# Kernel tuning notes

Measured on AMD Instinct MI355X. Metric: run time of the kernel, lower is better.

## Reference

```python
import jax, jax.numpy as jnp
import numpy as np

NUM_GRAPHS = 128

def _gcn_conv(x, W, b, src, dst, deg_inv_sqrt, n_nodes):
    # PyG GCNConv: h = X W; out[dst] += d^-1/2[src] * d^-1/2[dst] * h[src]; out += b
    h = x @ W
    norm = deg_inv_sqrt[src] * deg_inv_sqrt[dst]  # [E]
    msg = h[src] * norm[:, None]                  # [E, C]
    out = jax.ops.segment_sum(msg, dst, num_segments=n_nodes)
    return out + b


def setup_inputs() -> dict:
    key = jax.random.key(0)
    k1, k2, k3, k4, k5 = jax.random.split(key, 5)
    n_nodes, n_edges, c_in, c_hid = 50000, 800000, 256, 256
    x = jax.random.normal(k1, (n_nodes, c_in), dtype=jnp.float32)
    edge_index = jax.random.randint(k2, (2, n_edges), 0, n_nodes, dtype=jnp.int64)
    batch = jnp.sort(jax.random.randint(k3, (n_nodes,), 0, NUM_GRAPHS, dtype=jnp.int64))
    s1 = 1.0 / np.sqrt(c_in)
    s2 = 1.0 / np.sqrt(c_hid)
    W1 = jax.random.uniform(k4, (c_in, c_hid), jnp.float32, -s1, s1)
    b1 = jnp.zeros((c_hid,), jnp.float32)
    W2 = jax.random.uniform(k5, (c_hid, c_hid), jnp.float32, -s2, s2)
    b2 = jnp.zeros((c_hid,), jnp.float32)
    return {"x": x, "edge_index": edge_index, "batch": batch,
            "W1": W1, "b1": b1, "W2": W2, "b2": b2}


def reference(x, edge_index, batch, W1, b1, W2, b2):
    n_nodes = x.shape[0]
    # add self-loops (GCNConv default add_self_loops=True)
    loops = jnp.arange(n_nodes, dtype=edge_index.dtype)
    src = jnp.concatenate([edge_index[0], loops])
    dst = jnp.concatenate([edge_index[1], loops])
    deg = jax.ops.segment_sum(jnp.ones_like(dst, dtype=x.dtype), dst, num_segments=n_nodes)
    deg_inv_sqrt = jnp.where(deg > 0, jax.lax.rsqrt(deg), 0.0)

    h = jax.nn.relu(_gcn_conv(x, W1, b1, src, dst, deg_inv_sqrt, n_nodes))
    # dropout p=0.2 is identity in eval mode
    h = jax.nn.relu(_gcn_conv(h, W2, b2, src, dst, deg_inv_sqrt, n_nodes))

    # global mean pool over graph ids
    sums = jax.ops.segment_sum(h, batch, num_segments=NUM_GRAPHS)
    cnts = jax.ops.segment_sum(jnp.ones((n_nodes,), h.dtype), batch, num_segments=NUM_GRAPHS)
    return sums / jnp.maximum(cnts, 1.0)[:, None]
```

## Files before the change

### kernel.cpp

```cpp
#include <hip/hip_runtime.h>

#define NCH 256
#define NS  16

typedef short short8 __attribute__((ext_vector_type(8)));
typedef float f32x4  __attribute__((ext_vector_type(4)));

__device__ __forceinline__ float b2f(unsigned short u) {
    union { unsigned int i; float f; } x; x.i = ((unsigned int)u) << 16; return x.f;
}
__device__ __forceinline__ unsigned short f2b(float f) {
    unsigned int u = __float_as_uint(f);
    unsigned int r = (u + 0x7FFFu + ((u >> 16) & 1u)) >> 16;
    return (unsigned short)r;
}

__global__ __launch_bounds__(256) void k_hist(const int* __restrict__ dst, int E,
                                              int* __restrict__ deg) {
    int e = blockIdx.x * 256 + threadIdx.x;
    if (e < E) atomicAdd(&deg[dst[e]], 1);
}

__global__ __launch_bounds__(256) void k_scan_blk(const int* __restrict__ deg,
                                                  int* __restrict__ part,
                                                  int* __restrict__ bsum, int N) {
    __shared__ int sm[256];
    int t = threadIdx.x;
    int base = blockIdx.x * 1024 + t * 4;
    int v[4]; int s = 0;
#pragma unroll
    for (int j = 0; j < 4; ++j) {
        int i = base + j;
        int d = (i < N) ? deg[i] : 0;
        v[j] = d; s += d;
    }
    sm[t] = s; __syncthreads();
#pragma unroll
    for (int off = 1; off < 256; off <<= 1) {
        int u = (t >= off) ? sm[t - off] : 0;
        __syncthreads();
        sm[t] += u;
        __syncthreads();
    }
    int excl = sm[t] - s;
#pragma unroll
    for (int j = 0; j < 4; ++j) {
        int i = base + j;
        if (i < N) part[i] = excl;
        excl += v[j];
    }
    if (t == 255) bsum[blockIdx.x] = sm[255];
}

__global__ void k_scan_top(int* __restrict__ bsum, int nb, int* __restrict__ rowptr_end) {
    int t = threadIdx.x;
    int orig = (t < nb) ? bsum[t] : 0;
    int v = orig;
#pragma unroll
    for (int off = 1; off < 64; off <<= 1) {
        int u = __shfl_up(v, off, 64);
        if (t >= off) v += u;
    }
    if (t < nb) bsum[t] = v - orig;
    if (t == 63) *rowptr_end = v;
}

__global__ __launch_bounds__(256) void k_finalize(const int* __restrict__ deg,
                                                  int* __restrict__ row_ptr,
                                                  const int* __restrict__ boff,
                                                  int* __restrict__ cursor,
                                                  float* __restrict__ dinv, int N) {
    int i = blockIdx.x * 256 + threadIdx.x;
    if (i < N) {
        int rp = row_ptr[i] + boff[i >> 10];
        row_ptr[i] = rp;
        cursor[i]  = rp;
        dinv[i] = rsqrtf((float)(deg[i] + 1));
    }
}

__global__ __launch_bounds__(256) void k_scatter(const int* __restrict__ src,
                                                 const int* __restrict__ dst, int E,
                                                 int* __restrict__ cursor,
                                                 const float* __restrict__ dinv,
                                                 int2* __restrict__ cw) {
    int e = blockIdx.x * 256 + threadIdx.x;
    if (e < E) {
        int d = dst[e];
        int s = src[e];
        int pos = atomicAdd(&cursor[d], 1);
        cw[pos] = make_int2(s, __float_as_int(dinv[s]));
    }
}

__global__ __launch_bounds__(256) void k_castT(const float* __restrict__ W1,
                                               const float* __restrict__ W2,
                                               unsigned short* __restrict__ Wt1,
                                               unsigned short* __restrict__ Wt2) {
    int k = blockIdx.x, n = threadIdx.x;
    const float* W = blockIdx.y ? W2 : W1;
    unsigned short* Wt = blockIdx.y ? Wt2 : Wt1;
    Wt[(size_t)n * 256 + k] = f2b(W[(size_t)k * 256 + n]);
}

__device__ __forceinline__ void a_load_b(const unsigned short* __restrict__ A,
                                         int tile, int M, int lr, int ku, short8* dst) {
    int row = tile * 16 + lr; if (row >= M) row = M - 1;
    const unsigned short* pa = A + (size_t)row * NCH + ku * 8;
#pragma unroll
    for (int ks = 0; ks < 8; ++ks) dst[ks] = *(const short8*)(pa + ks * 32);
}

__device__ __forceinline__ void a_load_f(const float* __restrict__ A,
                                         int tile, int M, int lr, int ku, short8* dst) {
    int row = tile * 16 + lr; if (row >= M) row = M - 1;
    const float* pa = A + (size_t)row * NCH + ku * 8;
#pragma unroll
    for (int ks = 0; ks < 8; ++ks) {
        float4 f0 = *(const float4*)(pa + ks * 32);
        float4 f1 = *(const float4*)(pa + ks * 32 + 4);
        short8 v;
        v[0] = (short)f2b(f0.x); v[1] = (short)f2b(f0.y);
        v[2] = (short)f2b(f0.z); v[3] = (short)f2b(f0.w);
        v[4] = (short)f2b(f1.x); v[5] = (short)f2b(f1.y);
        v[6] = (short)f2b(f1.z); v[7] = (short)f2b(f1.w);
        dst[ks] = v;
    }
}

template <bool AF32>
__device__ __forceinline__ void gemm_body(const void* __restrict__ Av,
                                          const unsigned short* __restrict__ Bt,
                                          unsigned short* __restrict__ C, int M) {
    const int tid  = threadIdx.x;
    const int wid  = tid >> 6;
    const int lane = tid & 63;
    const int lr   = lane & 15;
    const int ku   = lane >> 4;

    short8 bfr[4][8];
    {
        const unsigned short* pb = Bt + (size_t)(wid * 64 + lr) * NCH + ku * 8;
#pragma unroll
        for (int nf = 0; nf < 4; ++nf)
#pragma unroll
            for (int ks = 0; ks < 8; ++ks)
                bfr[nf][ks] = *(const short8*)(pb + nf * 16 * NCH + ks * 32);
    }

    const int tiles = (M + 15) >> 4;
    int t = blockIdx.x;

    short8 afA[8], afB[8];
    if (t < tiles) {
        if (AF32) a_load_f((const float*)Av, t, M, lr, ku, afA);
        else      a_load_b((const unsigned short*)Av, t, M, lr, ku, afA);
    }

    for (; t < tiles; t += gridDim.x) {
        int tn = t + gridDim.x;
        if (tn < tiles) {
            if (AF32) a_load_f((const float*)Av, tn, M, lr, ku, afB);
            else      a_load_b((const unsigned short*)Av, tn, M, lr, ku, afB);
        }

        f32x4 acc[4];
#pragma unroll
        for (int nf = 0; nf < 4; ++nf) acc[nf] = (f32x4){0.f, 0.f, 0.f, 0.f};

#pragma unroll
        for (int ks = 0; ks < 8; ++ks)
#pragma unroll
            for (int nf = 0; nf < 4; ++nf)
                acc[nf] = __builtin_amdgcn_mfma_f32_16x16x32_bf16(bfr[nf][ks], afA[ks],
                                                                  acc[nf], 0, 0, 0);

        int row = t * 16 + lr;
        if (row < M) {
            unsigned short* pc = C + (size_t)row * NCH + wid * 64 + ku * 4;
#pragma unroll
            for (int nf = 0; nf < 4; ++nf) {
                unsigned short us[4];
                us[0] = f2b(acc[nf][0]); us[1] = f2b(acc[nf][1]);
                us[2] = f2b(acc[nf][2]); us[3] = f2b(acc[nf][3]);
                *(int2*)(pc + nf * 16) = *(const int2*)us;
            }
        }
#pragma unroll
        for (int ks = 0; ks < 8; ++ks) afA[ks] = afB[ks];
    }
}

__global__ __launch_bounds__(256, 2) void k_gemm_f32in(const float* __restrict__ A,
                                                       const unsigned short* __restrict__ Bt,
                                                       unsigned short* __restrict__ C, int M) {
    gemm_body<true>(A, Bt, C, M);
}

__global__ __launch_bounds__(256, 2) void k_gemm_rs(const unsigned short* __restrict__ A,
                                                    const unsigned short* __restrict__ Bt,
                                                    unsigned short* __restrict__ C, int M) {
    gemm_body<false>(A, Bt, C, M);
}

__global__ __launch_bounds__(256) void k_agg_w(const unsigned short* __restrict__ h,
                                               const float* __restrict__ dinv,
                                               const int* __restrict__ row_ptr,
                                               const int2* __restrict__ cw,
                                               const float* __restrict__ bias,
                                               unsigned short* __restrict__ out,
                                               int v0, int vend) {
    int v = v0 + blockIdx.x * 4 + (threadIdx.x >> 6);
    if (v >= vend) return;
    const int lane = threadIdx.x & 63;
    const int half = lane >> 5;
    const int cb   = (lane & 31) << 3;

    float acc[8] = {};
    float dv = dinv[v];

    short8 rs = {};
    if (half == 0) rs = *(const short8*)&h[(size_t)v * NCH + cb];

    int beg = row_ptr[v], end = row_ptr[v + 1];
    int i0 = beg + half * 2;

    short8 r0 = {}, r1 = {};
    float  w0 = 0.f, w1 = 0.f;
    bool b0 = i0 < end, b1 = i0 + 1 < end;
    if (b0) {
        int2 e = cw[i0];
        r0 = *(const short8*)&h[(size_t)e.x * NCH + cb];
        w0 = __int_as_float(e.y);
    }
    if (b1) {
        int2 e = cw[i0 + 1];
        r1 = *(const short8*)&h[(size_t)e.x * NCH + cb];
        w1 = __int_as_float(e.y);
    }

    while (b0) {
        int in = i0 + 4;
        bool n0 = in < end, n1 = in + 1 < end;
        short8 s0 = {}, s1 = {};
        float  x0 = 0.f, x1 = 0.f;
        if (n0) {
            int2 e = cw[in];
            s0 = *(const short8*)&h[(size_t)e.x * NCH + cb];
            x0 = __int_as_float(e.y);
        }
        if (n1) {
            int2 e = cw[in + 1];
            s1 = *(const short8*)&h[(size_t)e.x * NCH + cb];
            x1 = __int_as_float(e.y);
        }
#pragma unroll
        for (int i = 0; i < 8; ++i) acc[i] += w0 * b2f((unsigned short)r0[i]);
#pragma unroll
        for (int i = 0; i < 8; ++i) acc[i] += w1 * b2f((unsigned short)r1[i]);
        r0 = s0; r1 = s1; w0 = x0; w1 = x1; b0 = n0; b1 = n1; i0 = in;
    }

    if (half == 0) {
#pragma unroll
        for (int i = 0; i < 8; ++i) acc[i] += dv * b2f((unsigned short)rs[i]);
    }

#pragma unroll
    for (int i = 0; i < 8; ++i) acc[i] += __shfl_xor(acc[i], 32, 64);

    if (half == 0) {
        f32x4 bl = *(const f32x4*)&bias[cb];
        f32x4 bh = *(const f32x4*)&bias[cb + 4];
        unsigned short us[8];
#pragma unroll
        for (int i = 0; i < 8; ++i) {
            float b = (i < 4) ? bl[i] : bh[i - 4];
            us[i] = f2b(fmaxf(dv * acc[i] + b, 0.0f));
        }
        *(int4*)&out[(size_t)v * NCH + cb] = *(const int4*)us;
    }
}

__device__ __forceinline__ int lower_bound_i(const int* a, int n, int key) {
    int lo = 0, hi = n;
    while (lo < hi) {
        int mid = (lo + hi) >> 1;
        if (a[mid] < key) lo = mid + 1; else hi = mid;
    }
    return lo;
}

__global__ __launch_bounds__(64) void k_pool_a(const unsigned short* __restrict__ a,
                                               const int* __restrict__ batch,
                                               float* __restrict__ partial, int N) {
    int g = blockIdx.x, s = blockIdx.y;
    const int lane = threadIdx.x;
    const int half = lane >> 5;
    const int cb   = (lane & 31) << 3;

    int lo = lower_bound_i(batch, N, g);
    int hi = lower_bound_i(batch, N, g + 1);
    int cnt = hi - lo;
    int len = (cnt + NS - 1) / NS;
    int rlo = lo + s * len;
    int rhi = min(rlo + len, hi);

    float acc[8] = {};
    for (int r = rlo + half; r < rhi; r += 2) {
        short8 hv = *(const short8*)&a[(size_t)r * NCH + cb];
#pragma unroll
        for (int i = 0; i < 8; ++i) acc[i] += b2f((unsigned short)hv[i]);
    }
#pragma unroll
    for (int i = 0; i < 8; ++i) acc[i] += __shfl_xor(acc[i], 32, 64);

    if (half == 0) {
        float* p = partial + ((size_t)g * NS + s) * NCH + cb;
        *(f32x4*)p       = (f32x4){acc[0], acc[1], acc[2], acc[3]};
        *(f32x4*)(p + 4) = (f32x4){acc[4], acc[5], acc[6], acc[7]};
    }
}

__global__ __launch_bounds__(256) void k_pool_b(const float* __restrict__ partial,
                                                const int* __restrict__ batch,
                                                float* __restrict__ out, int N) {
    int g = blockIdx.x, ch = threadIdx.x;
    int lo = lower_bound_i(batch, N, g);
    int hi = lower_bound_i(batch, N, g + 1);
    float s = 0.0f;
#pragma unroll
    for (int k = 0; k < NS; ++k)
        s += partial[((size_t)g * NS + k) * NCH + ch];
    out[(size_t)g * NCH + ch] = s / (float)max(hi - lo, 1);
}

extern "C" void kernel_launch(void* const* d_in, const int* in_sizes, int n_in,
                              void* d_out, int out_size, void* d_ws, size_t ws_size,
                              hipStream_t stream) {
    const float* x     = (const float*)d_in[0];
    const int*   ei    = (const int*)d_in[1];
    const int*   batch = (const int*)d_in[2];
    const float* W1    = (const float*)d_in[3];
    const float* b1    = (const float*)d_in[4];
    const float* W2    = (const float*)d_in[5];
    const float* b2    = (const float*)d_in[6];
    float* out = (float*)d_out;

    const int M = in_sizes[0] / NCH;
    const int E = in_sizes[1] / 2;
    const int* src = ei;
    const int* dst = ei + E;

    char* w = (char*)d_ws;
    auto alloc = [&](size_t bytes) -> void* {
        void* p = (void*)w;
        w += (bytes + 255) & ~(size_t)255;
        return p;
    };
    int*   deg     = (int*)alloc((size_t)M * 4);
    float* dinv    = (float*)alloc((size_t)M * 4);
    int*   row_ptr = (int*)alloc((size_t)(M + 1) * 4);
    int*   cursor  = (int*)alloc((size_t)M * 4);
    int*   bsum    = (int*)alloc(64 * 4);
    int2*  cw      = (int2*)alloc((size_t)E * 8);
    unsigned short* bufP = (unsigned short*)alloc((size_t)M * NCH * 2);
    unsigned short* bufQ = (unsigned short*)alloc((size_t)M * NCH * 2);
    unsigned short* Wt1  = (unsigned short*)alloc((size_t)NCH * NCH * 2);
    unsigned short* Wt2  = (unsigned short*)alloc((size_t)NCH * NCH * 2);
    float* partial = (float*)alloc((size_t)128 * NS * NCH * 4);

    const int nb = (M + 1023) / 1024;

    k_castT<<<dim3(256, 2), 256, 0, stream>>>(W1, W2, Wt1, Wt2);

    hipMemsetAsync(deg, 0, (size_t)M * 4, stream);
    k_hist<<<(E + 255) / 256, 256, 0, stream>>>(dst, E, deg);
    k_scan_blk<<<nb, 256, 0, stream>>>(deg, row_ptr, bsum, M);
    k_scan_top<<<1, 64, 0, stream>>>(bsum, nb, row_ptr + M);
    k_finalize<<<(M + 255) / 256, 256, 0, stream>>>(deg, row_ptr, bsum, cursor, dinv, M);
    k_scatter<<<(E + 255) / 256, 256, 0, stream>>>(src, dst, E, cursor, dinv, cw);

    const int ggrid = 512;
    const int Mh = M / 2;
    const int agrid = (Mh + 3) / 4;

    k_gemm_f32in<<<ggrid, 256, 0, stream>>>(x, Wt1, bufP, M);
    k_agg_w<<<agrid, 256, 0, stream>>>(bufP, dinv, row_ptr, cw, b1, bufQ, 0, Mh);
    k_agg_w<<<(M - Mh + 3) / 4, 256, 0, stream>>>(bufP, dinv, row_ptr, cw, b1, bufQ, Mh, M);
    k_gemm_rs<<<ggrid, 256, 0, stream>>>(bufQ, Wt2, bufP, M);
    k_agg_w<<<agrid, 256, 0, stream>>>(bufP, dinv, row_ptr, cw, b2, bufQ, 0, Mh);
    k_agg_w<<<(M - Mh + 3) / 4, 256, 0, stream>>>(bufP, dinv, row_ptr, cw, b2, bufQ, Mh, M);
    k_pool_a<<<dim3(128, NS), 64, 0, stream>>>(bufQ, batch, partial, M);
    k_pool_b<<<128, 256, 0, stream>>>(partial, batch, out, M);
}
```

Measured before the change: 320.0 us.

## Shard CSR scatter by destination range and double-buffer GEMM A-tile loads

The edge scatter now runs as 2048 blocks. Each block scans one chunk of edges but writes only those whose destination falls in its eighth of the node range, with the shard picked by a multiply-high. The aim is to keep cursor atomics and cw writes for nearby destinations in the same blocks for better cache locality, at the cost of reading dst eight times. The GEMM loop is unrolled by two with two A-fragment buffers, prefetching the tile two strides ahead (clamped) to hide load latency. The GEMM grid also doubles to 1024 blocks.

Measured after the change: 374.7 us. +17.1%, slower.

```diff
diff --git a/kernel.cpp b/kernel.cpp
--- a/kernel.cpp
+++ b/kernel.cpp
@@ -79,17 +79,26 @@
     }
 }
 
-__global__ __launch_bounds__(256) void k_scatter(const int* __restrict__ src,
-                                                 const int* __restrict__ dst, int E,
-                                                 int* __restrict__ cursor,
-                                                 const float* __restrict__ dinv,
-                                                 int2* __restrict__ cw) {
-    int e = blockIdx.x * 256 + threadIdx.x;
-    if (e < E) {
+__global__ __launch_bounds__(256) void k_scatter_sh(const int* __restrict__ src,
+                                                    const int* __restrict__ dst, int E,
+                                                    int* __restrict__ cursor,
+                                                    const float* __restrict__ dinv,
+                                                    int2* __restrict__ cw,
+                                                    unsigned shmul) {
+    const int shard  = blockIdx.x & 7;
+    const int nchunk = gridDim.x >> 3;
+    const int chunk  = blockIdx.x >> 3;
+    const int per = (E + nchunk - 1) / nchunk;
+    const int e0 = chunk * per;
+    const int e1 = min(e0 + per, E);
+    for (int e = e0 + threadIdx.x; e < e1; e += 256) {
         int d = dst[e];
-        int s = src[e];
-        int pos = atomicAdd(&cursor[d], 1);
-        cw[pos] = make_int2(s, __float_as_int(dinv[s]));
+        int s = (int)__umulhi((unsigned)d, shmul);
+        if (s == shard) {
+            int sv = src[e];
+            int pos = atomicAdd(&cursor[d], 1);
+            cw[pos] = make_int2(sv, __float_as_int(dinv[sv]));
+        }
     }
 }
 
@@ -149,46 +158,49 @@
     }
 
     const int tiles = (M + 15) >> 4;
+    const int G = gridDim.x;
     int t = blockIdx.x;
 
-    short8 afA[8], afB[8];
-    if (t < tiles) {
-        if (AF32) a_load_f((const float*)Av, t, M, lr, ku, afA);
-        else      a_load_b((const unsigned short*)Av, t, M, lr, ku, afA);
-    }
-
-    for (; t < tiles; t += gridDim.x) {
-        int tn = t + gridDim.x;
-        if (tn < tiles) {
-            if (AF32) a_load_f((const float*)Av, tn, M, lr, ku, afB);
-            else      a_load_b((const unsigned short*)Av, tn, M, lr, ku, afB);
-        }
-
-        f32x4 acc[4];
-#pragma unroll
-        for (int nf = 0; nf < 4; ++nf) acc[nf] = (f32x4){0.f, 0.f, 0.f, 0.f};
-
-#pragma unroll
-        for (int ks = 0; ks < 8; ++ks)
-#pragma unroll
-            for (int nf = 0; nf < 4; ++nf)
-                acc[nf] = __builtin_amdgcn_mfma_f32_16x16x32_bf16(bfr[nf][ks], afA[ks],
-                                                                  acc[nf], 0, 0, 0);
-
-        int row = t * 16 + lr;
-        if (row < M) {
-            unsigned short* pc = C + (size_t)row * NCH + wid * 64 + ku * 4;
-#pragma unroll
-            for (int nf = 0; nf < 4; ++nf) {
-                unsigned short us[4];
-                us[0] = f2b(acc[nf][0]); us[1] = f2b(acc[nf][1]);
-                us[2] = f2b(acc[nf][2]); us[3] = f2b(acc[nf][3]);
-                *(int2*)(pc + nf * 16) = *(const int2*)us;
-            }
-        }
-#pragma unroll
-        for (int ks = 0; ks < 8; ++ks) afA[ks] = afB[ks];
-    }
+#define LD_TILE(tt, buf) do {                                              \
+        int _t = (tt); if (_t >= tiles) _t = tiles - 1;                    \
+        if (AF32) a_load_f((const float*)Av, _t, M, lr, ku, buf);          \
+        else      a_load_b((const unsigned short*)Av, _t, M, lr, ku, buf); \
+    } while (0)
+
+#define STEP(buf, tt) do {                                                  \
+        f32x4 acc[4];                                                       \
+        _Pragma("unroll")                                                   \
+        for (int nf = 0; nf < 4; ++nf) acc[nf] = (f32x4){0.f,0.f,0.f,0.f};  \
+        _Pragma("unroll")                                                   \
+        for (int ks = 0; ks < 8; ++ks)                                      \
+            _Pragma("unroll")                                               \
+            for (int nf = 0; nf < 4; ++nf)                                  \
+                acc[nf] = __builtin_amdgcn_mfma_f32_16x16x32_bf16(          \
+                    bfr[nf][ks], buf[ks], acc[nf], 0, 0, 0);                \
+        LD_TILE((tt) + 2 * G, buf);         \
+        int row = (tt) * 16 + lr;                                           \
+        if (row < M) {                                                      \
+            unsigned short* pc = C + (size_t)row * NCH + wid * 64 + ku * 4; \
+            _Pragma("unroll")                                               \
+            for (int nf = 0; nf < 4; ++nf) {                                \
+                unsigned short us[4];                                       \
+                us[0] = f2b(acc[nf][0]); us[1] = f2b(acc[nf][1]);           \
+                us[2] = f2b(acc[nf][2]); us[3] = f2b(acc[nf][3]);           \
+                *(int2*)(pc + nf * 16) = *(const int2*)us;                  \
+            }                                                               \
+        }                                                                   \
+    } while (0)
+
+    short8 b0[8], b1[8];
+    LD_TILE(t, b0);
+    LD_TILE(t + G, b1);
+
+    for (; t < tiles; t += 2 * G) {
+        STEP(b0, t);
+        STEP(b1, t + G);
+    }
+#undef STEP
+#undef LD_TILE
 }
 
 __global__ __launch_bounds__(256, 2) void k_gemm_f32in(const float* __restrict__ A,
@@ -371,6 +383,7 @@
     float* partial = (float*)alloc((size_t)128 * NS * NCH * 4);
 
     const int nb = (M + 1023) / 1024;
+    const unsigned shmul = (unsigned)(((8ull << 32) + M - 1) / (unsigned long long)M);
 
     k_castT<<<dim3(256, 2), 256, 0, stream>>>(W1, W2, Wt1, Wt2);
 
@@ -379,9 +392,9 @@
     k_scan_blk<<<nb, 256, 0, stream>>>(deg, row_ptr, bsum, M);
     k_scan_top<<<1, 64, 0, stream>>>(bsum, nb, row_ptr + M);
     k_finalize<<<(M + 255) / 256, 256, 0, stream>>>(deg, row_ptr, bsum, cursor, dinv, M);
-    k_scatter<<<(E + 255) / 256, 256, 0, stream>>>(src, dst, E, cursor, dinv, cw);
-
-    const int ggrid = 512;
+    k_scatter_sh<<<2048, 256, 0, stream>>>(src, dst, E, cursor, dinv, cw, shmul);
+
+    const int ggrid = 1024;
     const int Mh = M / 2;
     const int agrid = (Mh + 3) / 4;
 
```
